# Kernel tuning notes

Hardware: AMD Instinct MI355X
Metric: run time of the kernel (lower is better)

## Reference

```python
import jax, jax.numpy as jnp
import numpy as np
import math

B, S, D, H = 4, 2048, 1024, 16
DH = D // H  # per-head dim = 64
MASK_VAL = -1000000.0


def setup_inputs() -> dict:
    key = jax.random.key(0)
    ks = jax.random.split(key, 9)
    queries = jax.random.normal(ks[0], (B, S, D), dtype=jnp.float32)
    keys = jax.random.normal(ks[1], (B, S, D), dtype=jnp.float32)
    values = jax.random.normal(ks[2], (B, S, D), dtype=jnp.float32)
    valid_lens = jax.random.randint(ks[3], (B,), 0, S, dtype=jnp.int32)
    scale = 1.0 / math.sqrt(D)
    Wq = jax.random.normal(ks[4], (D, D), dtype=jnp.float32) * scale
    Wk = jax.random.normal(ks[5], (D, D), dtype=jnp.float32) * scale
    Wv = jax.random.normal(ks[6], (D, D), dtype=jnp.float32) * scale
    Wo = jax.random.normal(ks[7], (D, D), dtype=jnp.float32) * scale
    return {"queries": queries, "keys": keys, "values": values,
            "valid_lens": valid_lens, "Wq": Wq, "Wk": Wk, "Wv": Wv, "Wo": Wo}


def _split_heads(x):  # [B,S,D] -> [B,H,S,DH]
    b, s, _ = x.shape
    return x.reshape(b, s, H, DH).transpose(0, 2, 1, 3)


def reference(queries, keys, values, valid_lens, Wq, Wk, Wv, Wo):
    q = _split_heads(queries @ Wq)  # [B,H,S,DH]
    k = _split_heads(keys @ Wk)
    v = _split_heads(values @ Wv)
    scores = jnp.einsum('bhqd,bhkd->bhqk', q, k) / jnp.sqrt(jnp.float32(DH))
    # mask key positions >= valid_len[b] (sequence_mask with value=-1e6)
    key_pos = jnp.arange(S)  # [S]
    mask = key_pos[None, None, None, :] < valid_lens[:, None, None, None]  # [B,1,1,S]
    scores = jnp.where(mask, scores, MASK_VAL)
    attn = jax.nn.softmax(scores, axis=-1)  # [B,H,S,S] -- the 1GB intermediate
    out = jnp.einsum('bhqk,bhkd->bhqd', attn, v)  # [B,H,S,DH]
    out = out.transpose(0, 2, 1, 3).reshape(B, S, D)  # concat heads
    return out @ Wo
```

## Files before the change

### kernel.cpp

```cpp
#include <hip/hip_runtime.h>

#define BB 4
#define SS 2048
#define DD 1024
#define HH 16
#define DHH 64

typedef _Float16 half8 __attribute__((ext_vector_type(8)));
typedef _Float16 half4v __attribute__((ext_vector_type(4)));
typedef float floatx4 __attribute__((ext_vector_type(4)));

#define GLOBAL_AS __attribute__((address_space(1)))
#define LDS_AS __attribute__((address_space(3)))

__global__ void prep_kernel(const float* __restrict__ q, const float* __restrict__ k,
                            const float* __restrict__ v, const float* __restrict__ wq,
                            const float* __restrict__ wk, const float* __restrict__ wv,
                            const float* __restrict__ wo, _Float16* __restrict__ wt,
                            _Float16* __restrict__ acat) {
  int bx = blockIdx.x;
  if (bx < 4096) {
    __shared__ float tile[32][33];
    int z = bx >> 10, rem = bx & 1023;
    const float* w = (z == 0) ? wq : (z == 1) ? wk : (z == 2) ? wv : wo;
    float scale = (z == 0) ? 0.125f : 1.0f;
    _Float16* dst = wt + (size_t)z * 1048576;
    int k0 = (rem >> 5) * 32, n0 = (rem & 31) * 32;
    int tx = threadIdx.x & 31, ty = threadIdx.x >> 5;
#pragma unroll
    for (int r = ty; r < 32; r += 8) tile[r][tx] = w[(size_t)(k0 + r) * 1024 + n0 + tx];
    __syncthreads();
#pragma unroll
    for (int r = ty; r < 32; r += 8)
      dst[(size_t)(n0 + r) * 1024 + k0 + tx] = (_Float16)(tile[tx][r] * scale);
  } else {
    int idx = bx - 4096;
    int z = idx >> 12, xx = idx & 4095;
    const float* src = (z == 0) ? q : (z == 1) ? k : v;
    size_t i = ((size_t)xx * 256 + threadIdx.x) * 8;
    float4 f0 = *(const float4*)(src + i);
    float4 f1 = *(const float4*)(src + i + 4);
    half8 h = {(_Float16)f0.x, (_Float16)f0.y, (_Float16)f0.z, (_Float16)f0.w,
               (_Float16)f1.x, (_Float16)f1.y, (_Float16)f1.z, (_Float16)f1.w};
    *(half8*)(acat + (size_t)z * 8388608 + i) = h;
  }
}

__global__ __launch_bounds__(256) void qkv_gemm(const _Float16* __restrict__ Acat,
                                                const _Float16* __restrict__ Wt,
                                                _Float16* __restrict__ Qf,
                                                _Float16* __restrict__ Kf,
                                                _Float16* __restrict__ Vt) {
  __shared__ _Float16 lA[128 * 32];
  __shared__ _Float16 lB[128 * 32];
  int tid = threadIdx.x;
  int wave = tid >> 6, lane = tid & 63, quad = lane >> 4, l15 = lane & 15;
  int bn = blockIdx.x, bm = blockIdx.y;
  int proj = bm >> 6;
  int wm = wave >> 1, wn = wave & 1;

  const _Float16* A = Acat + (size_t)bm * 128 * 1024;
  const _Float16* W = Wt + (size_t)proj * 1024 * 1024;

  floatx4 fzero = {0.f, 0.f, 0.f, 0.f};
  floatx4 acc[4][4];
#pragma unroll
  for (int i = 0; i < 4; ++i)
#pragma unroll
    for (int j = 0; j < 4; ++j) acc[i][j] = fzero;

  int g0 = tid, g1 = 256 + tid;
  int row0 = g0 >> 2, gc0 = (g0 & 3) ^ ((row0 >> 1) & 3);
  int row1 = g1 >> 2, gc1 = (g1 & 3) ^ ((row1 >> 1) & 3);
  const _Float16* a0 = A + ((size_t)row0 * 1024 + gc0 * 8);
  const _Float16* a1 = A + ((size_t)row1 * 1024 + gc1 * 8);
  const _Float16* b0 = W + ((size_t)(bn * 128 + row0) * 1024 + gc0 * 8);
  const _Float16* b1 = W + ((size_t)(bn * 128 + row1) * 1024 + gc1 * 8);

  for (int k0 = 0; k0 < 1024; k0 += 32) {
    __builtin_amdgcn_global_load_lds((const GLOBAL_AS void*)(a0 + k0),
                                     (LDS_AS void*)(lA + g0 * 8), 16, 0, 0);
    __builtin_amdgcn_global_load_lds((const GLOBAL_AS void*)(a1 + k0),
                                     (LDS_AS void*)(lA + g1 * 8), 16, 0, 0);
    __builtin_amdgcn_global_load_lds((const GLOBAL_AS void*)(b0 + k0),
                                     (LDS_AS void*)(lB + g0 * 8), 16, 0, 0);
    __builtin_amdgcn_global_load_lds((const GLOBAL_AS void*)(b1 + k0),
                                     (LDS_AS void*)(lB + g1 * 8), 16, 0, 0);
    __syncthreads();

    half8 af[4], bf[4];
#pragma unroll
    for (int i = 0; i < 4; ++i) {
      int row = wm * 64 + i * 16 + l15;
      af[i] = *(const half8*)(lA + (row * 4 + (quad ^ ((row >> 1) & 3))) * 8);
    }
#pragma unroll
    for (int j = 0; j < 4; ++j) {
      int row = wn * 64 + j * 16 + l15;
      bf[j] = *(const half8*)(lB + (row * 4 + (quad ^ ((row >> 1) & 3))) * 8);
    }
#pragma unroll
    for (int i = 0; i < 4; ++i)
#pragma unroll
      for (int j = 0; j < 4; ++j)
        acc[i][j] = __builtin_amdgcn_mfma_f32_16x16x32_f16(af[i], bf[j], acc[i][j], 0, 0, 0);
    __syncthreads();
  }

  int rloc = (bm & 63) * 128;
#pragma unroll
  for (int i = 0; i < 4; ++i) {
#pragma unroll
    for (int j = 0; j < 4; ++j) {
      int rowb = rloc + wm * 64 + i * 16 + quad * 4;
      int col = bn * 128 + wn * 64 + j * 16 + l15;
      if (proj < 2) {
        _Float16* dst = (proj == 0) ? Qf : Kf;
#pragma unroll
        for (int r = 0; r < 4; ++r)
          dst[(size_t)(rowb + r) * 1024 + col] = (_Float16)acc[i][j][r];
      } else {
        int b = rowb >> 11, s = rowb & 2047;
        half4v pk = {(_Float16)acc[i][j][0], (_Float16)acc[i][j][1],
                     (_Float16)acc[i][j][2], (_Float16)acc[i][j][3]};
        *(half4v*)(Vt + (size_t)(b * 1024 + col) * 2048 + s) = pk;
      }
    }
  }
}

__global__ __launch_bounds__(256) void gemm_out(const _Float16* __restrict__ A,
                                                const _Float16* __restrict__ Wt,
                                                float* __restrict__ C) {
  __shared__ _Float16 lA[128 * 32];
  __shared__ _Float16 lB[128 * 32];
  int tid = threadIdx.x;
  int wave = tid >> 6, lane = tid & 63, quad = lane >> 4, l15 = lane & 15;
  int bn = blockIdx.x, bm = blockIdx.y;
  int wm = wave >> 1, wn = wave & 1;

  floatx4 fzero = {0.f, 0.f, 0.f, 0.f};
  floatx4 acc[4][4];
#pragma unroll
  for (int i = 0; i < 4; ++i)
#pragma unroll
    for (int j = 0; j < 4; ++j) acc[i][j] = fzero;

  int g0 = tid, g1 = 256 + tid;
  int row0 = g0 >> 2, gc0 = (g0 & 3) ^ ((row0 >> 1) & 3);
  int row1 = g1 >> 2, gc1 = (g1 & 3) ^ ((row1 >> 1) & 3);
  const _Float16* a0 = A + ((size_t)(bm * 128 + row0) * 1024 + gc0 * 8);
  const _Float16* a1 = A + ((size_t)(bm * 128 + row1) * 1024 + gc1 * 8);
  const _Float16* b0 = Wt + ((size_t)(bn * 128 + row0) * 1024 + gc0 * 8);
  const _Float16* b1 = Wt + ((size_t)(bn * 128 + row1) * 1024 + gc1 * 8);

  for (int k0 = 0; k0 < 1024; k0 += 32) {
    __builtin_amdgcn_global_load_lds((const GLOBAL_AS void*)(a0 + k0),
                                     (LDS_AS void*)(lA + g0 * 8), 16, 0, 0);
    __builtin_amdgcn_global_load_lds((const GLOBAL_AS void*)(a1 + k0),
                                     (LDS_AS void*)(lA + g1 * 8), 16, 0, 0);
    __builtin_amdgcn_global_load_lds((const GLOBAL_AS void*)(b0 + k0),
                                     (LDS_AS void*)(lB + g0 * 8), 16, 0, 0);
    __builtin_amdgcn_global_load_lds((const GLOBAL_AS void*)(b1 + k0),
                                     (LDS_AS void*)(lB + g1 * 8), 16, 0, 0);
    __syncthreads();

    half8 af[4], bf[4];
#pragma unroll
    for (int i = 0; i < 4; ++i) {
      int row = wm * 64 + i * 16 + l15;
      af[i] = *(const half8*)(lA + (row * 4 + (quad ^ ((row >> 1) & 3))) * 8);
    }
#pragma unroll
    for (int j = 0; j < 4; ++j) {
      int row = wn * 64 + j * 16 + l15;
      bf[j] = *(const half8*)(lB + (row * 4 + (quad ^ ((row >> 1) & 3))) * 8);
    }
#pragma unroll
    for (int i = 0; i < 4; ++i)
#pragma unroll
      for (int j = 0; j < 4; ++j)
        acc[i][j] = __builtin_amdgcn_mfma_f32_16x16x32_f16(af[i], bf[j], acc[i][j], 0, 0, 0);
    __syncthreads();
  }

#pragma unroll
  for (int i = 0; i < 4; ++i)
#pragma unroll
    for (int j = 0; j < 4; ++j) {
      int rowb = bm * 128 + wm * 64 + i * 16 + quad * 4;
      int col = bn * 128 + wn * 64 + j * 16 + l15;
#pragma unroll
      for (int r = 0; r < 4; ++r) C[(size_t)(rowb + r) * 1024 + col] = acc[i][j][r];
    }
}

__global__ __launch_bounds__(256) void attn_kernel(const _Float16* __restrict__ Q,
                                                   const _Float16* __restrict__ K,
                                                   const _Float16* __restrict__ Vt,
                                                   const int* __restrict__ vlens,
                                                   _Float16* __restrict__ O) {
  __shared__ _Float16 lK[64 * 64];
  __shared__ _Float16 lV[64 * 64];
  __shared__ _Float16 lP[4 * 16 * 64];

  int tid = threadIdx.x, wave = tid >> 6, lane = tid & 63, quad = lane >> 4, l15 = lane & 15;
  int bx = blockIdx.x;
  int b = bx & 3, h = blockIdx.y;
  int q0 = (bx >> 2) * 64;
  int vlen = vlens[b];
  int nch = (vlen == 0) ? (SS / 64) : ((vlen + 63) >> 6);
  float mask_val = (vlen == 0) ? 0.0f : -1.0e6f;

  const _Float16* qb = Q + ((size_t)(b * SS + q0 + wave * 16 + l15) * DD + h * 64 + quad * 8);
  half8 qf0 = *(const half8*)qb;
  half8 qf1 = *(const half8*)(qb + 32);

  int g0 = tid, g1 = tid + 256;
  int kr0 = g0 >> 3, kc0 = (g0 & 7) ^ (kr0 & 7);
  int kr1 = g1 >> 3, kc1 = (g1 & 7) ^ (kr1 & 7);
  const _Float16* ksrc0 = K + ((size_t)(b * SS + kr0) * DD + h * 64 + kc0 * 8);
  const _Float16* ksrc1 = K + ((size_t)(b * SS + kr1) * DD + h * 64 + kc1 * 8);
  const _Float16* vsrc0 = Vt + ((size_t)(b * DD + h * 64 + kr0) * SS + kc0 * 8);
  const _Float16* vsrc1 = Vt + ((size_t)(b * DD + h * 64 + kr1) * SS + kc1 * 8);

  float l_part[4] = {0.f, 0.f, 0.f, 0.f};
  floatx4 fzero = {0.f, 0.f, 0.f, 0.f};
  floatx4 o[4];
#pragma unroll
  for (int j = 0; j < 4; ++j) o[j] = fzero;

  for (int kc = 0; kc < nch; ++kc) {
    int kb = kc * 64;
    __builtin_amdgcn_global_load_lds((const GLOBAL_AS void*)(ksrc0 + (size_t)kb * DD),
                                     (LDS_AS void*)(lK + g0 * 8), 16, 0, 0);
    __builtin_amdgcn_global_load_lds((const GLOBAL_AS void*)(ksrc1 + (size_t)kb * DD),
                                     (LDS_AS void*)(lK + g1 * 8), 16, 0, 0);
    __builtin_amdgcn_global_load_lds((const GLOBAL_AS void*)(vsrc0 + kb),
                                     (LDS_AS void*)(lV + g0 * 8), 16, 0, 0);
    __builtin_amdgcn_global_load_lds((const GLOBAL_AS void*)(vsrc1 + kb),
                                     (LDS_AS void*)(lV + g1 * 8), 16, 0, 0);
    __syncthreads();

    floatx4 sacc[4];
#pragma unroll
    for (int j = 0; j < 4; ++j) sacc[j] = fzero;
#pragma unroll
    for (int ks = 0; ks < 2; ++ks) {
      half8 qf = ks ? qf1 : qf0;
#pragma unroll
      for (int j = 0; j < 4; ++j) {
        int row = j * 16 + l15, gc = ks * 4 + quad;
        half8 kf = *(const half8*)(lK + (row * 8 + (gc ^ (row & 7))) * 8);
        sacc[j] = __builtin_amdgcn_mfma_f32_16x16x32_f16(qf, kf, sacc[j], 0, 0, 0);
      }
    }

    bool clean = (kb + 64 <= vlen);
#pragma unroll
    for (int j = 0; j < 4; ++j) {
      int key = kb + j * 16 + l15;
      bool valid = clean | (key < vlen);
#pragma unroll
      for (int r = 0; r < 4; ++r) {
        float s = valid ? sacc[j][r] : mask_val;
        float p = __expf(s);
        l_part[r] += p;
        int row = quad * 4 + r, col = j * 16 + l15;
        int gc = col >> 3, off = col & 7;
        lP[wave * 1024 + row * 64 + (gc ^ (row & 7)) * 8 + off] = (_Float16)p;
      }
    }

#pragma unroll
    for (int ks = 0; ks < 2; ++ks) {
      int gc = ks * 4 + quad;
      half8 pf = *(const half8*)(lP + wave * 1024 + l15 * 64 + (gc ^ (l15 & 7)) * 8);
#pragma unroll
      for (int j = 0; j < 4; ++j) {
        int row = j * 16 + l15;
        half8 vf = *(const half8*)(lV + (row * 8 + (gc ^ (row & 7))) * 8);
        o[j] = __builtin_amdgcn_mfma_f32_16x16x32_f16(pf, vf, o[j], 0, 0, 0);
      }
    }
    __syncthreads();
  }

  float inv_l[4];
#pragma unroll
  for (int r = 0; r < 4; ++r) {
    float l = l_part[r];
#pragma unroll
    for (int off = 1; off < 16; off <<= 1) l += __shfl_xor(l, off);
    inv_l[r] = 1.0f / l;
  }
#pragma unroll
  for (int j = 0; j < 4; ++j) {
    int col = h * 64 + j * 16 + l15;
#pragma unroll
    for (int r = 0; r < 4; ++r) {
      int qrow = q0 + wave * 16 + quad * 4 + r;
      O[(size_t)(b * SS + qrow) * DD + col] = (_Float16)(o[j][r] * inv_l[r]);
    }
  }
}

extern "C" void kernel_launch(void* const* d_in, const int* in_sizes, int n_in,
                              void* d_out, int out_size, void* d_ws, size_t ws_size,
                              hipStream_t stream) {
  const float* q = (const float*)d_in[0];
  const float* k = (const float*)d_in[1];
  const float* v = (const float*)d_in[2];
  const int* vl = (const int*)d_in[3];
  const float* wq = (const float*)d_in[4];
  const float* wk = (const float*)d_in[5];
  const float* wv = (const float*)d_in[6];
  const float* wo = (const float*)d_in[7];

  char* ws = (char*)d_ws;
  _Float16* Wt = (_Float16*)ws;
  _Float16* Acat = (_Float16*)(ws + (8u << 20));
  _Float16* Qf = (_Float16*)(ws + (56u << 20));
  _Float16* Kf = (_Float16*)(ws + (72u << 20));
  _Float16* Vt = (_Float16*)(ws + (88u << 20));
  _Float16* Of = Acat;

  dim3 blk(256);

  prep_kernel<<<dim3(16384), blk, 0, stream>>>(q, k, v, wq, wk, wv, wo, Wt, Acat);
  qkv_gemm<<<dim3(8, 192), blk, 0, stream>>>(Acat, Wt, Qf, Kf, Vt);
  attn_kernel<<<dim3(128, 16), blk, 0, stream>>>(Qf, Kf, Vt, vl, Of);
  gemm_out<<<dim3(8, 64), blk, 0, stream>>>(Of, Wt + 3 * 1048576, (float*)d_out);
}
```

Baseline: 359.2 us.

## Fuse fp32-to-fp16 activation conversion into QKV GEMM and use register loads in attention

The separate pass that converts the fp32 query/key/value activations to an fp16 workspace buffer is removed. The QKV GEMM now reads fp32 rows directly, converts them in registers and stores them into LDS, so prep_kernel only transposes the weights. The attention kernel's K/V tile loads change from async global-to-LDS builtins to plain register loads followed by swizzled LDS stores. This saves a write and re-read of 48MB of fp16 activations, but the GEMM's A loads now pass through registers and are no longer async, which may expose load latency.

```diff
diff --git a/kernel.cpp b/kernel.cpp
--- a/kernel.cpp
+++ b/kernel.cpp
@@ -13,40 +13,28 @@
 #define GLOBAL_AS __attribute__((address_space(1)))
 #define LDS_AS __attribute__((address_space(3)))
 
-__global__ void prep_kernel(const float* __restrict__ q, const float* __restrict__ k,
-                            const float* __restrict__ v, const float* __restrict__ wq,
-                            const float* __restrict__ wk, const float* __restrict__ wv,
-                            const float* __restrict__ wo, _Float16* __restrict__ wt,
-                            _Float16* __restrict__ acat) {
+__global__ void prep_kernel(const float* __restrict__ wq, const float* __restrict__ wk,
+                            const float* __restrict__ wv, const float* __restrict__ wo,
+                            _Float16* __restrict__ wt) {
+  __shared__ float tile[32][33];
   int bx = blockIdx.x;
-  if (bx < 4096) {
-    __shared__ float tile[32][33];
-    int z = bx >> 10, rem = bx & 1023;
-    const float* w = (z == 0) ? wq : (z == 1) ? wk : (z == 2) ? wv : wo;
-    float scale = (z == 0) ? 0.125f : 1.0f;
-    _Float16* dst = wt + (size_t)z * 1048576;
-    int k0 = (rem >> 5) * 32, n0 = (rem & 31) * 32;
-    int tx = threadIdx.x & 31, ty = threadIdx.x >> 5;
-#pragma unroll
-    for (int r = ty; r < 32; r += 8) tile[r][tx] = w[(size_t)(k0 + r) * 1024 + n0 + tx];
-    __syncthreads();
-#pragma unroll
-    for (int r = ty; r < 32; r += 8)
-      dst[(size_t)(n0 + r) * 1024 + k0 + tx] = (_Float16)(tile[tx][r] * scale);
-  } else {
-    int idx = bx - 4096;
-    int z = idx >> 12, xx = idx & 4095;
-    const float* src = (z == 0) ? q : (z == 1) ? k : v;
-    size_t i = ((size_t)xx * 256 + threadIdx.x) * 8;
-    float4 f0 = *(const float4*)(src + i);
-    float4 f1 = *(const float4*)(src + i + 4);
-    half8 h = {(_Float16)f0.x, (_Float16)f0.y, (_Float16)f0.z, (_Float16)f0.w,
-               (_Float16)f1.x, (_Float16)f1.y, (_Float16)f1.z, (_Float16)f1.w};
-    *(half8*)(acat + (size_t)z * 8388608 + i) = h;
-  }
-}
-
-__global__ __launch_bounds__(256) void qkv_gemm(const _Float16* __restrict__ Acat,
+  int z = bx >> 10, rem = bx & 1023;
+  const float* w = (z == 0) ? wq : (z == 1) ? wk : (z == 2) ? wv : wo;
+  float scale = (z == 0) ? 0.125f : 1.0f;
+  _Float16* dst = wt + (size_t)z * 1048576;
+  int k0 = (rem >> 5) * 32, n0 = (rem & 31) * 32;
+  int tx = threadIdx.x & 31, ty = threadIdx.x >> 5;
+#pragma unroll
+  for (int r = ty; r < 32; r += 8) tile[r][tx] = w[(size_t)(k0 + r) * 1024 + n0 + tx];
+  __syncthreads();
+#pragma unroll
+  for (int r = ty; r < 32; r += 8)
+    dst[(size_t)(n0 + r) * 1024 + k0 + tx] = (_Float16)(tile[tx][r] * scale);
+}
+
+__global__ __launch_bounds__(256) void qkv_gemm(const float* __restrict__ q,
+                                                const float* __restrict__ k,
+                                                const float* __restrict__ v,
                                                 const _Float16* __restrict__ Wt,
                                                 _Float16* __restrict__ Qf,
                                                 _Float16* __restrict__ Kf,
@@ -59,8 +47,9 @@
   int proj = bm >> 6;
   int wm = wave >> 1, wn = wave & 1;
 
-  const _Float16* A = Acat + (size_t)bm * 128 * 1024;
-  const _Float16* W = Wt + (size_t)proj * 1024 * 1024;
+  const float* Asrc = (proj == 0) ? q : (proj == 1) ? k : v;
+  const _Float16* W = Wt + (size_t)proj * 1048576;
+  int rbase = (bm & 63) * 128;
 
   floatx4 fzero = {0.f, 0.f, 0.f, 0.f};
   floatx4 acc[4][4];
@@ -72,10 +61,94 @@
   int g0 = tid, g1 = 256 + tid;
   int row0 = g0 >> 2, gc0 = (g0 & 3) ^ ((row0 >> 1) & 3);
   int row1 = g1 >> 2, gc1 = (g1 & 3) ^ ((row1 >> 1) & 3);
-  const _Float16* a0 = A + ((size_t)row0 * 1024 + gc0 * 8);
-  const _Float16* a1 = A + ((size_t)row1 * 1024 + gc1 * 8);
+  const float* a0 = Asrc + ((size_t)(rbase + row0) * 1024 + gc0 * 8);
+  const float* a1 = Asrc + ((size_t)(rbase + row1) * 1024 + gc1 * 8);
   const _Float16* b0 = W + ((size_t)(bn * 128 + row0) * 1024 + gc0 * 8);
   const _Float16* b1 = W + ((size_t)(bn * 128 + row1) * 1024 + gc1 * 8);
+
+  for (int k0 = 0; k0 < 1024; k0 += 32) {
+    __builtin_amdgcn_global_load_lds((const GLOBAL_AS void*)(b0 + k0),
+                                     (LDS_AS void*)(lB + g0 * 8), 16, 0, 0);
+    __builtin_amdgcn_global_load_lds((const GLOBAL_AS void*)(b1 + k0),
+                                     (LDS_AS void*)(lB + g1 * 8), 16, 0, 0);
+    {
+      float4 f0 = *(const float4*)(a0 + k0);
+      float4 f1 = *(const float4*)(a0 + k0 + 4);
+      half8 h = {(_Float16)f0.x, (_Float16)f0.y, (_Float16)f0.z, (_Float16)f0.w,
+                 (_Float16)f1.x, (_Float16)f1.y, (_Float16)f1.z, (_Float16)f1.w};
+      *(half8*)(lA + g0 * 8) = h;
+      float4 f2 = *(const float4*)(a1 + k0);
+      float4 f3 = *(const float4*)(a1 + k0 + 4);
+      half8 h2 = {(_Float16)f2.x, (_Float16)f2.y, (_Float16)f2.z, (_Float16)f2.w,
+                  (_Float16)f3.x, (_Float16)f3.y, (_Float16)f3.z, (_Float16)f3.w};
+      *(half8*)(lA + g1 * 8) = h2;
+    }
+    __syncthreads();
+
+    half8 af[4], bf[4];
+#pragma unroll
+    for (int i = 0; i < 4; ++i) {
+      int row = wm * 64 + i * 16 + l15;
+      af[i] = *(const half8*)(lA + (row * 4 + (quad ^ ((row >> 1) & 3))) * 8);
+    }
+#pragma unroll
+    for (int j = 0; j < 4; ++j) {
+      int row = wn * 64 + j * 16 + l15;
+      bf[j] = *(const half8*)(lB + (row * 4 + (quad ^ ((row >> 1) & 3))) * 8);
+    }
+#pragma unroll
+    for (int i = 0; i < 4; ++i)
+#pragma unroll
+      for (int j = 0; j < 4; ++j)
+        acc[i][j] = __builtin_amdgcn_mfma_f32_16x16x32_f16(af[i], bf[j], acc[i][j], 0, 0, 0);
+    __syncthreads();
+  }
+
+#pragma unroll
+  for (int i = 0; i < 4; ++i) {
+#pragma unroll
+    for (int j = 0; j < 4; ++j) {
+      int rowb = rbase + wm * 64 + i * 16 + quad * 4;
+      int col = bn * 128 + wn * 64 + j * 16 + l15;
+      if (proj < 2) {
+        _Float16* dst = (proj == 0) ? Qf : Kf;
+#pragma unroll
+        for (int r = 0; r < 4; ++r)
+          dst[(size_t)(rowb + r) * 1024 + col] = (_Float16)acc[i][j][r];
+      } else {
+        int b = rowb >> 11, s = rowb & 2047;
+        half4v pk = {(_Float16)acc[i][j][0], (_Float16)acc[i][j][1],
+                     (_Float16)acc[i][j][2], (_Float16)acc[i][j][3]};
+        *(half4v*)(Vt + (size_t)(b * 1024 + col) * 2048 + s) = pk;
+      }
+    }
+  }
+}
+
+__global__ __launch_bounds__(256) void gemm_out(const _Float16* __restrict__ A,
+                                                const _Float16* __restrict__ Wt,
+                                                float* __restrict__ C) {
+  __shared__ _Float16 lA[128 * 32];
+  __shared__ _Float16 lB[128 * 32];
+  int tid = threadIdx.x;
+  int wave = tid >> 6, lane = tid & 63, quad = lane >> 4, l15 = lane & 15;
+  int bn = blockIdx.x, bm = blockIdx.y;
+  int wm = wave >> 1, wn = wave & 1;
+
+  floatx4 fzero = {0.f, 0.f, 0.f, 0.f};
+  floatx4 acc[4][4];
+#pragma unroll
+  for (int i = 0; i < 4; ++i)
+#pragma unroll
+    for (int j = 0; j < 4; ++j) acc[i][j] = fzero;
+
+  int g0 = tid, g1 = 256 + tid;
+  int row0 = g0 >> 2, gc0 = (g0 & 3) ^ ((row0 >> 1) & 3);
+  int row1 = g1 >> 2, gc1 = (g1 & 3) ^ ((row1 >> 1) & 3);
+  const _Float16* a0 = A + ((size_t)(bm * 128 + row0) * 1024 + gc0 * 8);
+  const _Float16* a1 = A + ((size_t)(bm * 128 + row1) * 1024 + gc1 * 8);
+  const _Float16* b0 = Wt + ((size_t)(bn * 128 + row0) * 1024 + gc0 * 8);
+  const _Float16* b1 = Wt + ((size_t)(bn * 128 + row1) * 1024 + gc1 * 8);
 
   for (int k0 = 0; k0 < 1024; k0 += 32) {
     __builtin_amdgcn_global_load_lds((const GLOBAL_AS void*)(a0 + k0),
@@ -107,83 +180,6 @@
     __syncthreads();
   }
 
-  int rloc = (bm & 63) * 128;
-#pragma unroll
-  for (int i = 0; i < 4; ++i) {
-#pragma unroll
-    for (int j = 0; j < 4; ++j) {
-      int rowb = rloc + wm * 64 + i * 16 + quad * 4;
-      int col = bn * 128 + wn * 64 + j * 16 + l15;
-      if (proj < 2) {
-        _Float16* dst = (proj == 0) ? Qf : Kf;
-#pragma unroll
-        for (int r = 0; r < 4; ++r)
-          dst[(size_t)(rowb + r) * 1024 + col] = (_Float16)acc[i][j][r];
-      } else {
-        int b = rowb >> 11, s = rowb & 2047;
-        half4v pk = {(_Float16)acc[i][j][0], (_Float16)acc[i][j][1],
-                     (_Float16)acc[i][j][2], (_Float16)acc[i][j][3]};
-        *(half4v*)(Vt + (size_t)(b * 1024 + col) * 2048 + s) = pk;
-      }
-    }
-  }
-}
-
-__global__ __launch_bounds__(256) void gemm_out(const _Float16* __restrict__ A,
-                                                const _Float16* __restrict__ Wt,
-                                                float* __restrict__ C) {
-  __shared__ _Float16 lA[128 * 32];
-  __shared__ _Float16 lB[128 * 32];
-  int tid = threadIdx.x;
-  int wave = tid >> 6, lane = tid & 63, quad = lane >> 4, l15 = lane & 15;
-  int bn = blockIdx.x, bm = blockIdx.y;
-  int wm = wave >> 1, wn = wave & 1;
-
-  floatx4 fzero = {0.f, 0.f, 0.f, 0.f};
-  floatx4 acc[4][4];
-#pragma unroll
-  for (int i = 0; i < 4; ++i)
-#pragma unroll
-    for (int j = 0; j < 4; ++j) acc[i][j] = fzero;
-
-  int g0 = tid, g1 = 256 + tid;
-  int row0 = g0 >> 2, gc0 = (g0 & 3) ^ ((row0 >> 1) & 3);
-  int row1 = g1 >> 2, gc1 = (g1 & 3) ^ ((row1 >> 1) & 3);
-  const _Float16* a0 = A + ((size_t)(bm * 128 + row0) * 1024 + gc0 * 8);
-  const _Float16* a1 = A + ((size_t)(bm * 128 + row1) * 1024 + gc1 * 8);
-  const _Float16* b0 = Wt + ((size_t)(bn * 128 + row0) * 1024 + gc0 * 8);
-  const _Float16* b1 = Wt + ((size_t)(bn * 128 + row1) * 1024 + gc1 * 8);
-
-  for (int k0 = 0; k0 < 1024; k0 += 32) {
-    __builtin_amdgcn_global_load_lds((const GLOBAL_AS void*)(a0 + k0),
-                                     (LDS_AS void*)(lA + g0 * 8), 16, 0, 0);
-    __builtin_amdgcn_global_load_lds((const GLOBAL_AS void*)(a1 + k0),
-                                     (LDS_AS void*)(lA + g1 * 8), 16, 0, 0);
-    __builtin_amdgcn_global_load_lds((const GLOBAL_AS void*)(b0 + k0),
-                                     (LDS_AS void*)(lB + g0 * 8), 16, 0, 0);
-    __builtin_amdgcn_global_load_lds((const GLOBAL_AS void*)(b1 + k0),
-                                     (LDS_AS void*)(lB + g1 * 8), 16, 0, 0);
-    __syncthreads();
-
-    half8 af[4], bf[4];
-#pragma unroll
-    for (int i = 0; i < 4; ++i) {
-      int row = wm * 64 + i * 16 + l15;
-      af[i] = *(const half8*)(lA + (row * 4 + (quad ^ ((row >> 1) & 3))) * 8);
-    }
-#pragma unroll
-    for (int j = 0; j < 4; ++j) {
-      int row = wn * 64 + j * 16 + l15;
-      bf[j] = *(const half8*)(lB + (row * 4 + (quad ^ ((row >> 1) & 3))) * 8);
-    }
-#pragma unroll
-    for (int i = 0; i < 4; ++i)
-#pragma unroll
-      for (int j = 0; j < 4; ++j)
-        acc[i][j] = __builtin_amdgcn_mfma_f32_16x16x32_f16(af[i], bf[j], acc[i][j], 0, 0, 0);
-    __syncthreads();
-  }
-
 #pragma unroll
   for (int i = 0; i < 4; ++i)
 #pragma unroll
@@ -216,14 +212,6 @@
   half8 qf0 = *(const half8*)qb;
   half8 qf1 = *(const half8*)(qb + 32);
 
-  int g0 = tid, g1 = tid + 256;
-  int kr0 = g0 >> 3, kc0 = (g0 & 7) ^ (kr0 & 7);
-  int kr1 = g1 >> 3, kc1 = (g1 & 7) ^ (kr1 & 7);
-  const _Float16* ksrc0 = K + ((size_t)(b * SS + kr0) * DD + h * 64 + kc0 * 8);
-  const _Float16* ksrc1 = K + ((size_t)(b * SS + kr1) * DD + h * 64 + kc1 * 8);
-  const _Float16* vsrc0 = Vt + ((size_t)(b * DD + h * 64 + kr0) * SS + kc0 * 8);
-  const _Float16* vsrc1 = Vt + ((size_t)(b * DD + h * 64 + kr1) * SS + kc1 * 8);
-
   float l_part[4] = {0.f, 0.f, 0.f, 0.f};
   floatx4 fzero = {0.f, 0.f, 0.f, 0.f};
   floatx4 o[4];
@@ -232,14 +220,15 @@
 
   for (int kc = 0; kc < nch; ++kc) {
     int kb = kc * 64;
-    __builtin_amdgcn_global_load_lds((const GLOBAL_AS void*)(ksrc0 + (size_t)kb * DD),
-                                     (LDS_AS void*)(lK + g0 * 8), 16, 0, 0);
-    __builtin_amdgcn_global_load_lds((const GLOBAL_AS void*)(ksrc1 + (size_t)kb * DD),
-                                     (LDS_AS void*)(lK + g1 * 8), 16, 0, 0);
-    __builtin_amdgcn_global_load_lds((const GLOBAL_AS void*)(vsrc0 + kb),
-                                     (LDS_AS void*)(lV + g0 * 8), 16, 0, 0);
-    __builtin_amdgcn_global_load_lds((const GLOBAL_AS void*)(vsrc1 + kb),
-                                     (LDS_AS void*)(lV + g1 * 8), 16, 0, 0);
+#pragma unroll
+    for (int ss = tid; ss < 512; ss += 256) {
+      int row = ss >> 3, gc = ss & 7;
+      int sidx = (row * 8 + (gc ^ (row & 7))) * 8;
+      *(half8*)(lK + sidx) =
+          *(const half8*)(K + ((size_t)(b * SS + kb + row) * DD + h * 64 + gc * 8));
+      *(half8*)(lV + sidx) =
+          *(const half8*)(Vt + ((size_t)(b * DD + h * 64 + row) * SS + kb + gc * 8));
+    }
     __syncthreads();
 
     floatx4 sacc[4];
@@ -319,16 +308,15 @@
 
   char* ws = (char*)d_ws;
   _Float16* Wt = (_Float16*)ws;
-  _Float16* Acat = (_Float16*)(ws + (8u << 20));
-  _Float16* Qf = (_Float16*)(ws + (56u << 20));
-  _Float16* Kf = (_Float16*)(ws + (72u << 20));
-  _Float16* Vt = (_Float16*)(ws + (88u << 20));
-  _Float16* Of = Acat;
+  _Float16* Qf = (_Float16*)(ws + (8u << 20));
+  _Float16* Kf = (_Float16*)(ws + (24u << 20));
+  _Float16* Vt = (_Float16*)(ws + (40u << 20));
+  _Float16* Of = (_Float16*)(ws + (56u << 20));
 
   dim3 blk(256);
 
-  prep_kernel<<<dim3(16384), blk, 0, stream>>>(q, k, v, wq, wk, wv, wo, Wt, Acat);
-  qkv_gemm<<<dim3(8, 192), blk, 0, stream>>>(Acat, Wt, Qf, Kf, Vt);
+  prep_kernel<<<dim3(4096), blk, 0, stream>>>(wq, wk, wv, wo, Wt);
+  qkv_gemm<<<dim3(8, 192), blk, 0, stream>>>(q, k, v, Wt, Qf, Kf, Vt);
   attn_kernel<<<dim3(128, 16), blk, 0, stream>>>(Qf, Kf, Vt, vl, Of);
   gemm_out<<<dim3(8, 64), blk, 0, stream>>>(Of, Wt + 3 * 1048576, (float*)d_out);
 }
```

Result: slower. 381.7 us (+6.3%).
